# Optimization experiments

Hardware: AMD Instinct MI355X
Metric: run time of the kernel (lower is better)

Reference implementation:

```python
import jax, jax.numpy as jnp
import numpy as np

T, B, D = 256, 256, 512
H, DK = 8, 64          # num_heads, d_kv; inner_dim = H*DK = 512
NUM_GROUPS = 16


def setup_inputs() -> dict:
    key = jax.random.key(0)
    ks = jax.random.split(key, 6)
    hidden_states = jax.random.normal(ks[0], (T, B, D), dtype=jnp.float32)
    # sorted group ids over the batch axis (what _infer_group_ids_from_mask recovers)
    group_ids = jnp.sort(jax.random.randint(ks[1], (B,), 0, NUM_GROUPS, dtype=jnp.int32))
    scale = 1.0 / np.sqrt(D)
    Wq = jax.random.normal(ks[2], (D, H * DK), dtype=jnp.float32) * scale
    Wk = jax.random.normal(ks[3], (D, H * DK), dtype=jnp.float32) * scale
    Wv = jax.random.normal(ks[4], (D, H * DK), dtype=jnp.float32) * scale
    Wo = jax.random.normal(ks[5], (H * DK, D), dtype=jnp.float32) * scale
    return {"hidden_states": hidden_states, "group_ids": group_ids,
            "Wq": Wq, "Wk": Wk, "Wv": Wv, "Wo": Wo}


def reference(hidden_states, group_ids, Wq, Wk, Wv, Wo):
    # Group-restricted self-attention along the batch axis, per time step & head.
    # Equivalent to the block-sparse MiniFlash kernel: entries attend only to
    # batch entries with the same group id.
    t, b, d = hidden_states.shape
    q = (hidden_states @ Wq).reshape(t, b, H, DK)
    k = (hidden_states @ Wk).reshape(t, b, H, DK)
    v = (hidden_states @ Wv).reshape(t, b, H, DK)
    sm_scale = 1.0 / np.sqrt(DK)
    # scores: [T, H, B, B] over the batch axis
    scores = jnp.einsum("tihd,tjhd->thij", q, k) * sm_scale
    allowed = group_ids[:, None] == group_ids[None, :]          # [B, B]
    neg = jnp.finfo(scores.dtype).min
    scores = jnp.where(allowed[None, None, :, :], scores, neg)
    attn = jax.nn.softmax(scores, axis=-1)
    out = jnp.einsum("thij,tjhd->tihd", attn, v).reshape(t, b, H * DK)
    return out @ Wo
```

## Files before the change

### kernel.cpp

```cpp
#include <hip/hip_runtime.h>
#include <hip/hip_bf16.h>

typedef __attribute__((ext_vector_type(8))) short short8;
typedef __attribute__((ext_vector_type(4))) short short4v;
typedef __attribute__((ext_vector_type(4))) float f32x4;

#define MFMA16(a, b, c) __builtin_amdgcn_mfma_f32_16x16x32_bf16(a, b, c, 0, 0, 0)

__device__ __forceinline__ unsigned short f2bf(float f) {
    union { __hip_bfloat16 h; unsigned short u; } v;
    v.h = __float2bfloat16(f);
    return v.u;
}

__device__ __forceinline__ short8 pack8(float4 a, float4 b) {
    short8 p;
    p[0] = (short)f2bf(a.x); p[1] = (short)f2bf(a.y);
    p[2] = (short)f2bf(a.z); p[3] = (short)f2bf(a.w);
    p[4] = (short)f2bf(b.x); p[5] = (short)f2bf(b.y);
    p[6] = (short)f2bf(b.z); p[7] = (short)f2bf(b.w);
    return p;
}

__device__ __forceinline__ int swz64(int row, int bytecol) {
    return row * 64 + ((bytecol ^ ((row & 7) << 4)) >> 1);
}
__device__ __forceinline__ int swz256(int row, int bytecol) {
    return row * 256 + ((bytecol ^ ((row & 7) << 4)) >> 1);
}

__global__ __launch_bounds__(256) void wprep(
    const float* __restrict__ Wq, const float* __restrict__ Wk,
    const float* __restrict__ Wv, const float* __restrict__ Wo,
    unsigned short* __restrict__ wt)
{
    __shared__ float tile[64][65];
    const int bid = blockIdx.x;
    const int m = bid >> 6, tb = bid & 63;
    const int kr = (tb >> 3) << 6, nc = (tb & 7) << 6;
    const float* W = (m == 0) ? Wq : (m == 1) ? Wk : (m == 2) ? Wv : Wo;
    const int tid = threadIdx.x;
    for (int i = tid; i < 4096; i += 256)
        tile[i >> 6][i & 63] = W[(size_t)(kr + (i >> 6)) * 512 + nc + (i & 63)];
    __syncthreads();
    unsigned short* dst = wt + (size_t)m * 262144;
    for (int i = tid; i < 4096; i += 256)
        dst[(size_t)(nc + (i >> 6)) * 512 + kr + (i & 63)] = f2bf(tile[i & 63][i >> 6]);
}

__global__ __launch_bounds__(1024, 4) void qkv_gemm2(
    const float* __restrict__ hs,
    const unsigned short* __restrict__ wt,
    unsigned short* __restrict__ qkvb)
{
    __shared__ unsigned short As[128 * 64];
    __shared__ unsigned short Bts[512 * 64];

    const int orig = blockIdx.x;
    const int wg = (orig & 7) * 192 + (orig >> 3);
    const int mb = wg / 3;
    const int nb = wg - mb * 3;

    const int tid  = threadIdx.x;
    const int lane = tid & 63;
    const int w    = tid >> 6;
    const int l15  = lane & 15;
    const int hi4  = lane >> 4;
    const int wr   = w >> 3;
    const int wc   = w & 7;

    f32x4 acc[4][4];
    #pragma unroll
    for (int mt = 0; mt < 4; ++mt)
        #pragma unroll
        for (int nt = 0; nt < 4; ++nt)
            acc[mt][nt] = (f32x4){0.f, 0.f, 0.f, 0.f};

    const int ar = tid >> 3, aq = tid & 7;
    const int bc = tid >> 1, bh = tid & 1;
    const float* __restrict__ asrc = hs + ((size_t)mb * 128 + ar) * 512 + aq * 8;
    const unsigned short* __restrict__ bsrc =
        wt + ((size_t)nb * 512 + bc) * 512 + bh * 32;

    float4 a0, a1;
    short8 b8[4];
    a0 = *(const float4*)asrc;
    a1 = *(const float4*)(asrc + 4);
    #pragma unroll
    for (int q = 0; q < 4; ++q) b8[q] = *(const short8*)(bsrc + q * 8);

    for (int kb = 0; kb < 512; kb += 64) {
        *(short8*)&As[swz64(ar, aq * 16)] = pack8(a0, a1);
        #pragma unroll
        for (int q = 0; q < 4; ++q)
            *(short8*)&Bts[swz64(bc, bh * 64 + q * 16)] = b8[q];
        __syncthreads();
        if (kb < 448) {
            const int kn = kb + 64;
            a0 = *(const float4*)(asrc + kn);
            a1 = *(const float4*)(asrc + kn + 4);
            #pragma unroll
            for (int q = 0; q < 4; ++q)
                b8[q] = *(const short8*)(bsrc + kn + q * 8);
        }
        #pragma unroll
        for (int ks = 0; ks < 2; ++ks) {
            short8 af[4];
            #pragma unroll
            for (int mt = 0; mt < 4; ++mt)
                af[mt] = *(const short8*)&As[swz64(wr * 64 + mt * 16 + l15,
                                                   ks * 64 + hi4 * 16)];
            __builtin_amdgcn_s_setprio(1);
            #pragma unroll
            for (int nt = 0; nt < 4; ++nt) {
                const short8 bf = *(const short8*)&Bts[swz64(wc * 64 + nt * 16 + l15,
                                                             ks * 64 + hi4 * 16)];
                #pragma unroll
                for (int mt = 0; mt < 4; ++mt)
                    acc[mt][nt] = MFMA16(af[mt], bf, acc[mt][nt]);
            }
            __builtin_amdgcn_s_setprio(0);
        }
        __syncthreads();
    }

    unsigned short* __restrict__ dst = qkvb + (size_t)nb * 33554432ull;
    #pragma unroll
    for (int mt = 0; mt < 4; ++mt) {
        #pragma unroll
        for (int nt = 0; nt < 4; ++nt) {
            const int col = wc * 64 + nt * 16 + l15;
            #pragma unroll
            for (int r = 0; r < 4; ++r) {
                const int row = mb * 128 + wr * 64 + mt * 16 + hi4 * 4 + r;
                dst[(size_t)row * 512 + col] = f2bf(acc[mt][nt][r]);
            }
        }
    }
}

__global__ __launch_bounds__(1024, 4) void attn_split(
    const unsigned short* __restrict__ qkvb,
    const int* __restrict__ gid,
    unsigned short* __restrict__ abuf,
    float* __restrict__ out)
{
    __shared__ unsigned short Ksh[256 * 64];
    __shared__ unsigned short Vt[64 * 256];
    __shared__ unsigned short Ps[256 * 64];
    __shared__ int sgid[256];
    __shared__ int glo[16], ghi[16];

    const int th = blockIdx.x;
    const int t = th >> 3, h = th & 7;
    const int tid  = threadIdx.x;
    const int lane = tid & 63;
    const int w    = tid >> 6;
    const int l15  = lane & 15;
    const int hi4  = lane >> 4;
    const int wrow = w << 4;

    if (tid < 16) { glo[tid] = 256; ghi[tid] = -1; }
    __syncthreads();
    if (tid < 256) {
        const int g = gid[tid];
        sgid[tid] = g;
        atomicMin(&glo[g], tid);
        atomicMax(&ghi[g], tid);
    }

    const size_t rowbase = (size_t)t * 256 * 512 + h * 64;
    const unsigned short* __restrict__ qb = qkvb + rowbase;
    const unsigned short* __restrict__ kbp = qkvb + 33554432ull + rowbase;
    const unsigned short* __restrict__ vbp = qkvb + 67108864ull + rowbase;

    {
        const int kr = tid >> 2, kq = tid & 3;
        const short8 k0 = *(const short8*)(kbp + (size_t)kr * 512 + kq * 16);
        const short8 k1 = *(const short8*)(kbp + (size_t)kr * 512 + kq * 16 + 8);
        *(short8*)&Ksh[swz64(kr, kq * 32)]      = k0;
        *(short8*)&Ksh[swz64(kr, kq * 32 + 16)] = k1;
        const short8 v0 = *(const short8*)(vbp + (size_t)kr * 512 + kq * 16);
        const short8 v1 = *(const short8*)(vbp + (size_t)kr * 512 + kq * 16 + 8);
        *(short8*)&Ps[kr * 64 + kq * 16]     = v0;
        *(short8*)&Ps[kr * 64 + kq * 16 + 8] = v1;
    }
    short8 qf[2];
    #pragma unroll
    for (int ks = 0; ks < 2; ++ks)
        qf[ks] = *(const short8*)(qb + (size_t)(wrow + l15) * 512 + ks * 32 + hi4 * 8);
    __syncthreads();

    {
        const int d = tid & 63, jc = tid >> 6;
        short8 a, b;
        #pragma unroll
        for (int jj = 0; jj < 8; ++jj) a[jj] = Ps[(jc * 16 + jj) * 64 + d];
        #pragma unroll
        for (int jj = 0; jj < 8; ++jj) b[jj] = Ps[(jc * 16 + 8 + jj) * 64 + d];
        *(short8*)&Vt[swz256(d, jc * 32)]      = a;
        *(short8*)&Vt[swz256(d, jc * 32 + 16)] = b;
    }
    __syncthreads();

    int rg[4];
    #pragma unroll
    for (int r = 0; r < 4; ++r) rg[r] = sgid[wrow + hi4 * 4 + r];
    const int klo = glo[sgid[wrow]];
    const int khi = ghi[sgid[wrow + 15]];

    f32x4 o[4];
    float mrun[4], lrun[4];
    #pragma unroll
    for (int n = 0; n < 4; ++n) o[n] = (f32x4){0.f, 0.f, 0.f, 0.f};
    #pragma unroll
    for (int r = 0; r < 4; ++r) { mrun[r] = -3.0e38f; lrun[r] = 0.f; }

    for (int kc = klo & ~63; kc <= khi; kc += 64) {
        f32x4 sfr[4];
        __builtin_amdgcn_s_setprio(1);
        #pragma unroll
        for (int n = 0; n < 4; ++n) {
            const int krow = kc + n * 16 + l15;
            const short8 kf0 = *(const short8*)&Ksh[swz64(krow, hi4 * 16)];
            const short8 kf1 = *(const short8*)&Ksh[swz64(krow, 64 + hi4 * 16)];
            f32x4 z = (f32x4){0.f, 0.f, 0.f, 0.f};
            z = MFMA16(qf[0], kf0, z);
            z = MFMA16(qf[1], kf1, z);
            sfr[n] = z;
        }
        __builtin_amdgcn_s_setprio(0);
        int cg[4];
        #pragma unroll
        for (int n = 0; n < 4; ++n) cg[n] = sgid[kc + n * 16 + l15];

        #pragma unroll
        for (int r = 0; r < 4; ++r) {
            const int gr = rg[r];
            float sv[4];
            float smax = -3.0e38f;
            #pragma unroll
            for (int n = 0; n < 4; ++n) {
                float x = sfr[n][r] * 0.125f;
                x = (cg[n] == gr) ? x : -3.0e38f;
                sv[n] = x;
                smax = fmaxf(smax, x);
            }
            smax = fmaxf(smax, __shfl_xor(smax, 1));
            smax = fmaxf(smax, __shfl_xor(smax, 2));
            smax = fmaxf(smax, __shfl_xor(smax, 4));
            smax = fmaxf(smax, __shfl_xor(smax, 8));
            const float newm = fmaxf(mrun[r], smax);
            const float corr = __expf(mrun[r] - newm);
            float ps = 0.f;
            unsigned short pb[4];
            #pragma unroll
            for (int n = 0; n < 4; ++n) {
                const float p = (sv[n] > -1.0e38f) ? __expf(sv[n] - newm) : 0.f;
                ps += p;
                pb[n] = f2bf(p);
            }
            ps += __shfl_xor(ps, 1); ps += __shfl_xor(ps, 2);
            ps += __shfl_xor(ps, 4); ps += __shfl_xor(ps, 8);
            lrun[r] = lrun[r] * corr + ps;
            mrun[r] = newm;
            #pragma unroll
            for (int n = 0; n < 4; ++n) o[n][r] *= corr;
            const int prow = wrow + hi4 * 4 + r;
            #pragma unroll
            for (int n = 0; n < 4; ++n)
                Ps[swz64(prow, (n * 16 + l15) * 2)] = pb[n];
        }

        const short8 pa0 = *(const short8*)&Ps[swz64(wrow + l15, hi4 * 16)];
        const short8 pa1 = *(const short8*)&Ps[swz64(wrow + l15, 64 + hi4 * 16)];
        __builtin_amdgcn_s_setprio(1);
        #pragma unroll
        for (int n = 0; n < 4; ++n) {
            const short8 vb0 = *(const short8*)&Vt[swz256(n * 16 + l15, (kc + hi4 * 8) * 2)];
            const short8 vb1 = *(const short8*)&Vt[swz256(n * 16 + l15, (kc + 32 + hi4 * 8) * 2)];
            o[n] = MFMA16(pa0, vb0, o[n]);
            o[n] = MFMA16(pa1, vb1, o[n]);
        }
        __builtin_amdgcn_s_setprio(0);
    }

    if (abuf) {
        unsigned short* __restrict__ op = abuf + rowbase;
        #pragma unroll
        for (int r = 0; r < 4; ++r) {
            const int row = wrow + hi4 * 4 + r;
            const float inv = 1.0f / lrun[r];
            #pragma unroll
            for (int n = 0; n < 4; ++n)
                op[(size_t)row * 512 + n * 16 + l15] = f2bf(o[n][r] * inv);
        }
    } else {
        float* __restrict__ op = out + rowbase;
        #pragma unroll
        for (int r = 0; r < 4; ++r) {
            const int row = wrow + hi4 * 4 + r;
            const float inv = 1.0f / lrun[r];
            #pragma unroll
            for (int n = 0; n < 4; ++n)
                op[(size_t)row * 512 + n * 16 + l15] = o[n][r] * inv;
        }
    }
}

__global__ __launch_bounds__(1024, 4) void qkv_attn_mfma(
    const float* __restrict__ hs,
    const int*   __restrict__ gid,
    const float* __restrict__ Wq, const float* __restrict__ Wk,
    const float* __restrict__ Wv,
    const unsigned short* __restrict__ wt,
    float*       __restrict__ out)
{
    __shared__ unsigned short Xs[256 * 64];
    __shared__ unsigned short Wsh[192 * 64];
    __shared__ unsigned short Ksh[256 * 64];
    __shared__ unsigned short Vt[64 * 256];
    __shared__ unsigned short XP[256 * 64];
    __shared__ int sgid[256];
    __shared__ int glo[16], ghi[16];

    const int bid = blockIdx.x;
    const int h   = (bid & 63) >> 3;
    const int t   = ((bid >> 6) << 3) + (bid & 7);

    const int tid  = threadIdx.x;
    const int lane = tid & 63;
    const int w    = tid >> 6;
    const int l15  = lane & 15;
    const int hi4  = lane >> 4;
    const int mg   = w & 3;
    const int ng   = w >> 2;

    if (tid < 16) { glo[tid] = 256; ghi[tid] = -1; }
    __syncthreads();
    if (tid < 256) {
        const int g = gid[tid];
        sgid[tid] = g;
        atomicMin(&glo[g], tid);
        atomicMax(&ghi[g], tid);
    }

    const float* __restrict__ Xbase = hs + (size_t)t * (256 * 512);

    const int xr = tid >> 2, xq = tid & 3;
    const bool doW = tid < 768;
    const int wc = tid >> 2;
    const int wq = tid & 3;
    const int wmat = wc >> 6, wcol = wc & 63;
    const unsigned short* __restrict__ wsrc =
        wt ? wt + ((size_t)wmat * 512 + h * 64 + wcol) * 512 : nullptr;
    const float* __restrict__ wfsrc =
        (wmat == 0) ? Wq : (wmat == 1) ? Wk : Wv;

    f32x4 acc[4][3];
    #pragma unroll
    for (int mt = 0; mt < 4; ++mt)
        #pragma unroll
        for (int nt = 0; nt < 3; ++nt)
            acc[mt][nt] = (f32x4){0.f, 0.f, 0.f, 0.f};

    float4 xf[4];
    short8 w8[2];
    {
        const float* s = Xbase + (size_t)xr * 512 + xq * 16;
        xf[0] = *(const float4*)(s + 0);  xf[1] = *(const float4*)(s + 4);
        xf[2] = *(const float4*)(s + 8);  xf[3] = *(const float4*)(s + 12);
        if (doW) {
            if (wt) {
                w8[0] = *(const short8*)(wsrc + wq * 16);
                w8[1] = *(const short8*)(wsrc + wq * 16 + 8);
            } else {
                #pragma unroll
                for (int b = 0; b < 2; ++b)
                    #pragma unroll
                    for (int j = 0; j < 8; ++j)
                        w8[b][j] = (short)f2bf(
                            wfsrc[(size_t)(wq * 16 + b * 8 + j) * 512 + h * 64 + wcol]);
            }
        }
    }

    for (int kb = 0; kb < 512; kb += 64) {
        *(short8*)&Xs[swz64(xr, xq * 32 + 0)]  = pack8(xf[0], xf[1]);
        *(short8*)&Xs[swz64(xr, xq * 32 + 16)] = pack8(xf[2], xf[3]);
        if (doW) {
            *(short8*)&Wsh[swz64(wc, wq * 32 + 0)]  = w8[0];
            *(short8*)&Wsh[swz64(wc, wq * 32 + 16)] = w8[1];
        }
        __syncthreads();
        if (kb < 448) {
            const int kn = kb + 64;
            const float* s = Xbase + (size_t)xr * 512 + kn + xq * 16;
            xf[0] = *(const float4*)(s + 0);  xf[1] = *(const float4*)(s + 4);
            xf[2] = *(const float4*)(s + 8);  xf[3] = *(const float4*)(s + 12);
            if (doW) {
                if (wt) {
                    w8[0] = *(const short8*)(wsrc + kn + wq * 16);
                    w8[1] = *(const short8*)(wsrc + kn + wq * 16 + 8);
                } else {
                    #pragma unroll
                    for (int b = 0; b < 2; ++b)
                        #pragma unroll
                        for (int j = 0; j < 8; ++j)
                            w8[b][j] = (short)f2bf(
                                wfsrc[(size_t)(kn + wq * 16 + b * 8 + j) * 512 + h * 64 + wcol]);
                }
            }
        }
        #pragma unroll
        for (int ks = 0; ks < 2; ++ks) {
            short8 af[4];
            #pragma unroll
            for (int mt = 0; mt < 4; ++mt)
                af[mt] = *(const short8*)&Xs[swz64(mg * 64 + mt * 16 + l15,
                                                   ks * 64 + hi4 * 16)];
            __builtin_amdgcn_s_setprio(1);
            #pragma unroll
            for (int nt = 0; nt < 3; ++nt) {
                const short8 bf = *(const short8*)&Wsh[swz64(ng * 48 + nt * 16 + l15,
                                                             ks * 64 + hi4 * 16)];
                #pragma unroll
                for (int mt = 0; mt < 4; ++mt)
                    acc[mt][nt] = MFMA16(af[mt], bf, acc[mt][nt]);
            }
            __builtin_amdgcn_s_setprio(0);
        }
        __syncthreads();
    }

    #pragma unroll
    for (int nt = 0; nt < 3; ++nt) {
        const int c0 = (ng * 3 + nt) * 16;
        const int m  = c0 >> 6;
        const int d0 = c0 & 63;
        #pragma unroll
        for (int mt = 0; mt < 4; ++mt) {
            const int rowb = mg * 64 + mt * 16 + hi4 * 4;
            if (m == 0) {
                #pragma unroll
                for (int r = 0; r < 4; ++r)
                    XP[swz64(rowb + r, (d0 + l15) * 2)] = f2bf(acc[mt][nt][r]);
            } else if (m == 1) {
                #pragma unroll
                for (int r = 0; r < 4; ++r)
                    Ksh[swz64(rowb + r, (d0 + l15) * 2)] = f2bf(acc[mt][nt][r]);
            } else {
                short4v vv;
                #pragma unroll
                for (int r = 0; r < 4; ++r) vv[r] = (short)f2bf(acc[mt][nt][r]);
                *(short4v*)&Vt[swz256(d0 + l15, rowb * 2)] = vv;
            }
        }
    }
    __syncthreads();

    const int wrow = w << 4;
    int rg[4];
    #pragma unroll
    for (int r = 0; r < 4; ++r) rg[r] = sgid[wrow + hi4 * 4 + r];
    const int klo = glo[sgid[wrow]];
    const int khi = ghi[sgid[wrow + 15]];

    short8 qf[2];
    #pragma unroll
    for (int ks = 0; ks < 2; ++ks)
        qf[ks] = *(const short8*)&XP[swz64(wrow + l15, ks * 64 + hi4 * 16)];

    f32x4 o[4];
    float mrun[4], lrun[4];
    #pragma unroll
    for (int n = 0; n < 4; ++n) o[n] = (f32x4){0.f, 0.f, 0.f, 0.f};
    #pragma unroll
    for (int r = 0; r < 4; ++r) { mrun[r] = -3.0e38f; lrun[r] = 0.f; }

    for (int kc = klo & ~63; kc <= khi; kc += 64) {
        f32x4 sfr[4];
        __builtin_amdgcn_s_setprio(1);
        #pragma unroll
        for (int n = 0; n < 4; ++n) {
            const int krow = kc + n * 16 + l15;
            const short8 kf0 = *(const short8*)&Ksh[swz64(krow, hi4 * 16)];
            const short8 kf1 = *(const short8*)&Ksh[swz64(krow, 64 + hi4 * 16)];
            f32x4 z = (f32x4){0.f, 0.f, 0.f, 0.f};
            z = MFMA16(qf[0], kf0, z);
            z = MFMA16(qf[1], kf1, z);
            sfr[n] = z;
        }
        __builtin_amdgcn_s_setprio(0);
        int cg[4];
        #pragma unroll
        for (int n = 0; n < 4; ++n) cg[n] = sgid[kc + n * 16 + l15];

        #pragma unroll
        for (int r = 0; r < 4; ++r) {
            const int gr = rg[r];
            float sv[4];
            float smax = -3.0e38f;
            #pragma unroll
            for (int n = 0; n < 4; ++n) {
                float x = sfr[n][r] * 0.125f;
                x = (cg[n] == gr) ? x : -3.0e38f;
                sv[n] = x;
                smax = fmaxf(smax, x);
            }
            smax = fmaxf(smax, __shfl_xor(smax, 1));
            smax = fmaxf(smax, __shfl_xor(smax, 2));
            smax = fmaxf(smax, __shfl_xor(smax, 4));
            smax = fmaxf(smax, __shfl_xor(smax, 8));
            const float newm = fmaxf(mrun[r], smax);
            const float corr = __expf(mrun[r] - newm);
            float ps = 0.f;
            unsigned short pb[4];
            #pragma unroll
            for (int n = 0; n < 4; ++n) {
                const float p = (sv[n] > -1.0e38f) ? __expf(sv[n] - newm) : 0.f;
                ps += p;
                pb[n] = f2bf(p);
            }
            ps += __shfl_xor(ps, 1); ps += __shfl_xor(ps, 2);
            ps += __shfl_xor(ps, 4); ps += __shfl_xor(ps, 8);
            lrun[r] = lrun[r] * corr + ps;
            mrun[r] = newm;
            #pragma unroll
            for (int n = 0; n < 4; ++n) o[n][r] *= corr;
            const int prow = wrow + hi4 * 4 + r;
            #pragma unroll
            for (int n = 0; n < 4; ++n)
                XP[swz64(prow, (n * 16 + l15) * 2)] = pb[n];
        }

        const short8 pa0 = *(const short8*)&XP[swz64(wrow + l15, hi4 * 16)];
        const short8 pa1 = *(const short8*)&XP[swz64(wrow + l15, 64 + hi4 * 16)];
        __builtin_amdgcn_s_setprio(1);
        #pragma unroll
        for (int n = 0; n < 4; ++n) {
            const short8 vb0 = *(const short8*)&Vt[swz256(n * 16 + l15, (kc + hi4 * 8) * 2)];
            const short8 vb1 = *(const short8*)&Vt[swz256(n * 16 + l15, (kc + 32 + hi4 * 8) * 2)];
            o[n] = MFMA16(pa0, vb0, o[n]);
            o[n] = MFMA16(pa1, vb1, o[n]);
        }
        __builtin_amdgcn_s_setprio(0);
    }

    float* __restrict__ op = out + (size_t)t * (256 * 512) + h * 64;
    #pragma unroll
    for (int r = 0; r < 4; ++r) {
        const int row = wrow + hi4 * 4 + r;
        const float inv = 1.0f / lrun[r];
        #pragma unroll
        for (int n = 0; n < 4; ++n)
            op[(size_t)row * 512 + n * 16 + l15] = o[n][r] * inv;
    }
}

__global__ __launch_bounds__(1024, 4) void oproj_mfma(
    const float* __restrict__ Wo,
    const unsigned short* __restrict__ wot,
    const unsigned short* __restrict__ abuf,
    float* __restrict__ out)
{
    __shared__ unsigned short As[128 * 40];
    __shared__ unsigned short Bts[512 * 40];

    const int tid  = threadIdx.x;
    const int lane = tid & 63;
    const int w    = tid >> 6;
    const int l15  = lane & 15;
    const int hi4  = lane >> 4;
    const int wr   = w >> 2;
    const int wc   = w & 3;
    const size_t r0 = (size_t)blockIdx.x * 128;

    f32x4 acc[2][8];
    #pragma unroll
    for (int m = 0; m < 2; ++m)
        #pragma unroll
        for (int n = 0; n < 8; ++n)
            acc[m][n] = (f32x4){0.f, 0.f, 0.f, 0.f};

    const bool isA = tid < 512;
    const int bn = tid & 511;
    const int ai = bn >> 2, aq = bn & 3;

    float4 af0, af1;
    short8 a8;
    short8 b8[4];

    if (isA) {
        if (abuf) {
            a8 = *(const short8*)(abuf + (r0 + ai) * 512 + aq * 8);
        } else {
            const float* s = out + (r0 + ai) * 512 + aq * 8;
            af0 = *(const float4*)s; af1 = *(const float4*)(s + 4);
        }
    } else {
        if (wot) {
            #pragma unroll
            for (int q = 0; q < 4; ++q)
                b8[q] = *(const short8*)(wot + (size_t)bn * 512 + q * 8);
        } else {
            #pragma unroll
            for (int q = 0; q < 4; ++q)
                #pragma unroll
                for (int j = 0; j < 8; ++j)
                    b8[q][j] = (short)f2bf(Wo[(size_t)(q * 8 + j) * 512 + bn]);
        }
    }

    for (int kb = 0; kb < 512; kb += 32) {
        if (isA) *(short8*)&As[ai * 40 + aq * 8] = abuf ? a8 : pack8(af0, af1);
        else {
            #pragma unroll
            for (int q = 0; q < 4; ++q)
                *(short8*)&Bts[bn * 40 + q * 8] = b8[q];
        }
        __syncthreads();
        if (kb < 480) {
            const int kn = kb + 32;
            if (isA) {
                if (abuf) {
                    a8 = *(const short8*)(abuf + (r0 + ai) * 512 + kn + aq * 8);
                } else {
                    const float* s = out + (r0 + ai) * 512 + kn + aq * 8;
                    af0 = *(const float4*)s; af1 = *(const float4*)(s + 4);
                }
            } else {
                if (wot) {
                    #pragma unroll
                    for (int q = 0; q < 4; ++q)
                        b8[q] = *(const short8*)(wot + (size_t)bn * 512 + kn + q * 8);
                } else {
                    #pragma unroll
                    for (int q = 0; q < 4; ++q)
                        #pragma unroll
                        for (int j = 0; j < 8; ++j)
                            b8[q][j] = (short)f2bf(Wo[(size_t)(kn + q * 8 + j) * 512 + bn]);
                }
            }
        }
        short8 afr[2];
        #pragma unroll
        for (int m = 0; m < 2; ++m)
            afr[m] = *(const short8*)&As[(wr * 32 + m * 16 + l15) * 40 + hi4 * 8];
        __builtin_amdgcn_s_setprio(1);
        #pragma unroll
        for (int n = 0; n < 8; ++n) {
            const short8 bfr = *(const short8*)&Bts[(wc * 128 + n * 16 + l15) * 40 + hi4 * 8];
            #pragma unroll
            for (int m = 0; m < 2; ++m)
                acc[m][n] = MFMA16(afr[m], bfr, acc[m][n]);
        }
        __builtin_amdgcn_s_setprio(0);
        __syncthreads();
    }

    #pragma unroll
    for (int m = 0; m < 2; ++m)
        #pragma unroll
        for (int n = 0; n < 8; ++n)
            #pragma unroll
            for (int r = 0; r < 4; ++r)
                out[(r0 + wr * 32 + m * 16 + hi4 * 4 + r) * 512 + wc * 128 + n * 16 + l15] =
                    acc[m][n][r];
}

extern "C" void kernel_launch(void* const* d_in, const int* in_sizes, int n_in,
                              void* d_out, int out_size, void* d_ws, size_t ws_size,
                              hipStream_t stream) {
    const float* hs  = (const float*)d_in[0];
    const int*   gid = (const int*)  d_in[1];
    const float* Wq  = (const float*)d_in[2];
    const float* Wk  = (const float*)d_in[3];
    const float* Wv  = (const float*)d_in[4];
    const float* Wo  = (const float*)d_in[5];
    float* outp = (float*)d_out;

    const size_t WT_S  = 1048576;
    const size_t QKV_S = 100663296;
    const size_t AB_S  = 33554432;
    unsigned short* wt   = nullptr;
    unsigned short* wot  = nullptr;
    unsigned short* qkvb = nullptr;
    unsigned short* abuf = nullptr;
    if (ws_size >= WT_S * 2) {
        wt  = (unsigned short*)d_ws;
        wot = wt + (size_t)3 * 262144;
        wprep<<<256, 256, 0, stream>>>(Wq, Wk, Wv, Wo, wt);
        if (ws_size >= (WT_S + QKV_S) * 2)
            qkvb = wt + WT_S;
        if (ws_size >= (WT_S + QKV_S + AB_S) * 2)
            abuf = wt + WT_S + QKV_S;
    }

    if (qkvb) {
        qkv_gemm2<<<1536, 1024, 0, stream>>>(hs, wt, qkvb);
        attn_split<<<2048, 1024, 0, stream>>>(qkvb, gid, abuf, outp);
    } else {
        qkv_attn_mfma<<<2048, 1024, 0, stream>>>(hs, gid, Wq, Wk, Wv, wt, outp);
    }
    oproj_mfma<<<512, 1024, 0, stream>>>(Wo, wot, abuf, outp);
}
```

Measured before the change: 351.8 us.

## Add pre-swizzled bf16 inputs and direct-to-LDS async GEMMs for QKV and output projection

Adds an xprep kernel that converts hidden states to bf16 with an XOR swizzle baked into global memory, and makes wprep emit weights in the same layout. New 256-thread gemm_glds kernels use global_load_lds to copy tiles straight into LDS, so the projections no longer convert in registers or stage through VGPRs. The attention output is written swizzled in place over the Q buffer and feeds the same GEMM for the output projection. This adds an extra conversion pass over the hidden states and a larger workspace, and the GEMM main loop has no double buffering.

```diff
diff --git a/kernel.cpp b/kernel.cpp
--- a/kernel.cpp
+++ b/kernel.cpp
@@ -29,10 +29,17 @@
     return row * 256 + ((bytecol ^ ((row & 7) << 4)) >> 1);
 }
 
+__device__ __forceinline__ void async16(void* lds_uniform, const void* gsrc) {
+    __builtin_amdgcn_global_load_lds(
+        (const __attribute__((address_space(1))) unsigned int*)gsrc,
+        (__attribute__((address_space(3))) unsigned int*)lds_uniform,
+        16, 0, 0);
+}
+
 __global__ __launch_bounds__(256) void wprep(
     const float* __restrict__ Wq, const float* __restrict__ Wk,
     const float* __restrict__ Wv, const float* __restrict__ Wo,
-    unsigned short* __restrict__ wt)
+    unsigned short* __restrict__ wt, int swz)
 {
     __shared__ float tile[64][65];
     const int bid = blockIdx.x;
@@ -44,8 +51,115 @@
         tile[i >> 6][i & 63] = W[(size_t)(kr + (i >> 6)) * 512 + nc + (i & 63)];
     __syncthreads();
     unsigned short* dst = wt + (size_t)m * 262144;
-    for (int i = tid; i < 4096; i += 256)
-        dst[(size_t)(nc + (i >> 6)) * 512 + kr + (i & 63)] = f2bf(tile[i & 63][i >> 6]);
+    for (int i = tid; i < 4096; i += 256) {
+        const int n = nc + (i >> 6);
+        const int e = i & 63;
+        const int rsw = swz ? ((n & 7) * 8) : 0;
+        dst[(size_t)n * 512 + kr + e] = f2bf(tile[e ^ rsw][i >> 6]);
+    }
+}
+
+__global__ __launch_bounds__(256) void xprep(
+    const float* __restrict__ hs, unsigned short* __restrict__ xb)
+{
+    const long long total = 4194304;
+    for (long long g = (long long)blockIdx.x * 256 + threadIdx.x; g < total;
+         g += (long long)gridDim.x * 256) {
+        const int row = (int)(g >> 6);
+        const int e0  = ((int)g & 63) * 8;
+        const int src = e0 ^ ((row & 7) * 8);
+        const float* s = hs + (size_t)row * 512 + src;
+        const float4 f0 = *(const float4*)s;
+        const float4 f1 = *(const float4*)(s + 4);
+        *(short8*)(xb + (size_t)row * 512 + e0) = pack8(f0, f1);
+    }
+}
+
+template<int F32OUT>
+__global__ __launch_bounds__(256) void gemm_glds(
+    const unsigned short* __restrict__ A,
+    const unsigned short* __restrict__ B,
+    unsigned short* __restrict__ obf,
+    float* __restrict__ of32,
+    int nbcnt)
+{
+    __shared__ unsigned short As[128 * 64];
+    __shared__ unsigned short Bs[128 * 64];
+
+    const int orig  = blockIdx.x;
+    const int chunk = gridDim.x >> 3;
+    const int wg = (orig & 7) * chunk + (orig >> 3);
+    const int mb = wg / nbcnt;
+    const int nb = wg - mb * nbcnt;
+
+    const int tid  = threadIdx.x;
+    const int lane = tid & 63;
+    const int w    = tid >> 6;
+    const int l15  = lane & 15;
+    const int hi4  = lane >> 4;
+    const int wr   = w >> 1, wc = w & 1;
+
+    f32x4 acc[4][4];
+    #pragma unroll
+    for (int mt = 0; mt < 4; ++mt)
+        #pragma unroll
+        for (int nt = 0; nt < 4; ++nt)
+            acc[mt][nt] = (f32x4){0.f, 0.f, 0.f, 0.f};
+
+    const char* __restrict__ Ab = (const char*)(A + (size_t)mb * 128 * 512);
+    const char* __restrict__ Bb = (const char*)(B + (size_t)nb * 128 * 512);
+    const int sbase = w * 4096;
+
+    for (int kb = 0; kb < 512; kb += 64) {
+        #pragma unroll
+        for (int i = 0; i < 4; ++i) {
+            const int sb = sbase + i * 1024;
+            const int s  = sb + lane * 16;
+            const int row = s >> 7, colb = s & 127;
+            const size_t goff = (size_t)row * 1024 + kb * 2 + colb;
+            async16(&As[sb >> 1], Ab + goff);
+            async16(&Bs[sb >> 1], Bb + goff);
+        }
+        __syncthreads();
+        #pragma unroll
+        for (int ks = 0; ks < 2; ++ks) {
+            short8 af[4];
+            #pragma unroll
+            for (int mt = 0; mt < 4; ++mt)
+                af[mt] = *(const short8*)&As[swz64(wr * 64 + mt * 16 + l15,
+                                                   ks * 64 + hi4 * 16)];
+            __builtin_amdgcn_s_setprio(1);
+            #pragma unroll
+            for (int nt = 0; nt < 4; ++nt) {
+                const short8 bf = *(const short8*)&Bs[swz64(wc * 64 + nt * 16 + l15,
+                                                            ks * 64 + hi4 * 16)];
+                #pragma unroll
+                for (int mt = 0; mt < 4; ++mt)
+                    acc[mt][nt] = MFMA16(af[mt], bf, acc[mt][nt]);
+            }
+            __builtin_amdgcn_s_setprio(0);
+        }
+        __syncthreads();
+    }
+
+    #pragma unroll
+    for (int mt = 0; mt < 4; ++mt) {
+        #pragma unroll
+        for (int nt = 0; nt < 4; ++nt) {
+            const int colt = nb * 128 + wc * 64 + nt * 16 + l15;
+            #pragma unroll
+            for (int r = 0; r < 4; ++r) {
+                const int row = mb * 128 + wr * 64 + mt * 16 + hi4 * 4 + r;
+                if (F32OUT) {
+                    of32[(size_t)row * 512 + colt] = acc[mt][nt][r];
+                } else {
+                    const int mat = colt >> 9, cc = colt & 511;
+                    obf[(size_t)mat * 33554432 + (size_t)row * 512 + cc] =
+                        f2bf(acc[mt][nt][r]);
+                }
+            }
+        }
+    }
 }
 
 __global__ __launch_bounds__(1024, 4) void qkv_gemm2(
@@ -140,10 +254,9 @@
 }
 
 __global__ __launch_bounds__(1024, 4) void attn_split(
-    const unsigned short* __restrict__ qkvb,
+    unsigned short* __restrict__ qkvb,
     const int* __restrict__ gid,
-    unsigned short* __restrict__ abuf,
-    float* __restrict__ out)
+    int doswz)
 {
     __shared__ unsigned short Ksh[256 * 64];
     __shared__ unsigned short Vt[64 * 256];
@@ -170,7 +283,7 @@
     }
 
     const size_t rowbase = (size_t)t * 256 * 512 + h * 64;
-    const unsigned short* __restrict__ qb = qkvb + rowbase;
+    unsigned short* __restrict__ qb = qkvb + rowbase;
     const unsigned short* __restrict__ kbp = qkvb + 33554432ull + rowbase;
     const unsigned short* __restrict__ vbp = qkvb + 67108864ull + rowbase;
 
@@ -285,25 +398,15 @@
         __builtin_amdgcn_s_setprio(0);
     }
 
-    if (abuf) {
-        unsigned short* __restrict__ op = abuf + rowbase;
-        #pragma unroll
-        for (int r = 0; r < 4; ++r) {
-            const int row = wrow + hi4 * 4 + r;
-            const float inv = 1.0f / lrun[r];
-            #pragma unroll
-            for (int n = 0; n < 4; ++n)
-                op[(size_t)row * 512 + n * 16 + l15] = f2bf(o[n][r] * inv);
-        }
-    } else {
-        float* __restrict__ op = out + rowbase;
-        #pragma unroll
-        for (int r = 0; r < 4; ++r) {
-            const int row = wrow + hi4 * 4 + r;
-            const float inv = 1.0f / lrun[r];
-            #pragma unroll
-            for (int n = 0; n < 4; ++n)
-                op[(size_t)row * 512 + n * 16 + l15] = o[n][r] * inv;
+    #pragma unroll
+    for (int r = 0; r < 4; ++r) {
+        const int row = wrow + hi4 * 4 + r;
+        const float inv = 1.0f / lrun[r];
+        const int rsw = doswz ? ((row & 7) * 8) : 0;
+        #pragma unroll
+        for (int n = 0; n < 4; ++n) {
+            const int cc = n * 16 + l15;
+            qb[(size_t)row * 512 + (cc ^ rsw)] = f2bf(o[n][r] * inv);
         }
     }
 }
@@ -313,7 +416,6 @@
     const int*   __restrict__ gid,
     const float* __restrict__ Wq, const float* __restrict__ Wk,
     const float* __restrict__ Wv,
-    const unsigned short* __restrict__ wt,
     float*       __restrict__ out)
 {
     __shared__ unsigned short Xs[256 * 64];
@@ -352,8 +454,6 @@
     const int wc = tid >> 2;
     const int wq = tid & 3;
     const int wmat = wc >> 6, wcol = wc & 63;
-    const unsigned short* __restrict__ wsrc =
-        wt ? wt + ((size_t)wmat * 512 + h * 64 + wcol) * 512 : nullptr;
     const float* __restrict__ wfsrc =
         (wmat == 0) ? Wq : (wmat == 1) ? Wk : Wv;
 
@@ -371,17 +471,12 @@
         xf[0] = *(const float4*)(s + 0);  xf[1] = *(const float4*)(s + 4);
         xf[2] = *(const float4*)(s + 8);  xf[3] = *(const float4*)(s + 12);
         if (doW) {
-            if (wt) {
-                w8[0] = *(const short8*)(wsrc + wq * 16);
-                w8[1] = *(const short8*)(wsrc + wq * 16 + 8);
-            } else {
-                #pragma unroll
-                for (int b = 0; b < 2; ++b)
-                    #pragma unroll
-                    for (int j = 0; j < 8; ++j)
-                        w8[b][j] = (short)f2bf(
-                            wfsrc[(size_t)(wq * 16 + b * 8 + j) * 512 + h * 64 + wcol]);
-            }
+            #pragma unroll
+            for (int b = 0; b < 2; ++b)
+                #pragma unroll
+                for (int j = 0; j < 8; ++j)
+                    w8[b][j] = (short)f2bf(
+                        wfsrc[(size_t)(wq * 16 + b * 8 + j) * 512 + h * 64 + wcol]);
         }
     }
 
@@ -399,17 +494,12 @@
             xf[0] = *(const float4*)(s + 0);  xf[1] = *(const float4*)(s + 4);
             xf[2] = *(const float4*)(s + 8);  xf[3] = *(const float4*)(s + 12);
             if (doW) {
-                if (wt) {
-                    w8[0] = *(const short8*)(wsrc + kn + wq * 16);
-                    w8[1] = *(const short8*)(wsrc + kn + wq * 16 + 8);
-                } else {
+                #pragma unroll
+                for (int b = 0; b < 2; ++b)
                     #pragma unroll
-                    for (int b = 0; b < 2; ++b)
-                        #pragma unroll
-                        for (int j = 0; j < 8; ++j)
-                            w8[b][j] = (short)f2bf(
-                                wfsrc[(size_t)(kn + wq * 16 + b * 8 + j) * 512 + h * 64 + wcol]);
-                }
+                    for (int j = 0; j < 8; ++j)
+                        w8[b][j] = (short)f2bf(
+                            wfsrc[(size_t)(kn + wq * 16 + b * 8 + j) * 512 + h * 64 + wcol]);
             }
         }
         #pragma unroll
@@ -681,27 +771,27 @@
     float* outp = (float*)d_out;
 
     const size_t WT_S  = 1048576;
+    const size_t XB_S  = 33554432;
     const size_t QKV_S = 100663296;
-    const size_t AB_S  = 33554432;
-    unsigned short* wt   = nullptr;
-    unsigned short* wot  = nullptr;
-    unsigned short* qkvb = nullptr;
-    unsigned short* abuf = nullptr;
-    if (ws_size >= WT_S * 2) {
-        wt  = (unsigned short*)d_ws;
-        wot = wt + (size_t)3 * 262144;
-        wprep<<<256, 256, 0, stream>>>(Wq, Wk, Wv, Wo, wt);
-        if (ws_size >= (WT_S + QKV_S) * 2)
-            qkvb = wt + WT_S;
-        if (ws_size >= (WT_S + QKV_S + AB_S) * 2)
-            abuf = wt + WT_S + QKV_S;
-    }
-
-    if (qkvb) {
+    unsigned short* wt = (unsigned short*)d_ws;
+    unsigned short* wot = wt + (size_t)3 * 262144;
+
+    if (ws_size >= (WT_S + XB_S + QKV_S) * 2) {
+        unsigned short* xb   = wt + WT_S;
+        unsigned short* qkvb = xb + XB_S;
+        wprep<<<256, 256, 0, stream>>>(Wq, Wk, Wv, Wo, wt, 1);
+        xprep<<<2048, 256, 0, stream>>>(hs, xb);
+        gemm_glds<0><<<6144, 256, 0, stream>>>(xb, wt, qkvb, nullptr, 12);
+        attn_split<<<2048, 1024, 0, stream>>>(qkvb, gid, 1);
+        gemm_glds<1><<<2048, 256, 0, stream>>>(qkvb, wot, nullptr, outp, 4);
+    } else if (ws_size >= (WT_S + QKV_S) * 2) {
+        unsigned short* qkvb = wt + WT_S;
+        wprep<<<256, 256, 0, stream>>>(Wq, Wk, Wv, Wo, wt, 0);
         qkv_gemm2<<<1536, 1024, 0, stream>>>(hs, wt, qkvb);
-        attn_split<<<2048, 1024, 0, stream>>>(qkvb, gid, abuf, outp);
+        attn_split<<<2048, 1024, 0, stream>>>(qkvb, gid, 0);
+        oproj_mfma<<<512, 1024, 0, stream>>>(Wo, wot, qkvb, outp);
     } else {
-        qkv_attn_mfma<<<2048, 1024, 0, stream>>>(hs, gid, Wq, Wk, Wv, wt, outp);
-    }
-    oproj_mfma<<<512, 1024, 0, stream>>>(Wo, wot, abuf, outp);
-}
+        qkv_attn_mfma<<<2048, 1024, 0, stream>>>(hs, gid, Wq, Wk, Wv, outp);
+        oproj_mfma<<<512, 1024, 0, stream>>>(Wo, nullptr, nullptr, outp);
+    }
+}
```

Measured after the change: 341.1 us. 3.0% less time.
